# Optimization experiments

Hardware: AMD Instinct MI355X
Metric: run time of the kernel (lower is better)

## Reference

```python
import jax, jax.numpy as jnp
import numpy as np

D_MODEL = 1024
N_HEADS = 16
D_HEAD = D_MODEL // N_HEADS
CHUNK = 128
DECAY_RATE = 0.9


def setup_inputs() -> dict:
    key = jax.random.key(0)
    ks = jax.random.split(key, 10)
    B, L, D = 4, 4096, D_MODEL
    s = 1.0 / np.sqrt(D)
    return {
        "x": jax.random.normal(ks[0], (B, L, D), dtype=jnp.float32),
        "Wq": jax.random.normal(ks[1], (D, D), dtype=jnp.float32) * s,
        "bq": jnp.zeros((D,), dtype=jnp.float32),
        "Wk": jax.random.normal(ks[2], (D, D), dtype=jnp.float32) * s,
        "bk": jnp.zeros((D,), dtype=jnp.float32),
        "Wv": jax.random.normal(ks[3], (D, D), dtype=jnp.float32) * s,
        "bv": jnp.zeros((D,), dtype=jnp.float32),
        "Wo": jax.random.normal(ks[4], (D, D), dtype=jnp.float32) * s,
        "bo": jnp.zeros((D,), dtype=jnp.float32),
        "decay": jnp.full((N_HEADS,), DECAY_RATE, dtype=jnp.float32),
    }


def _retention(x, Wq, bq, Wk, bk, Wv, bv, Wo, bo, decay):
    B, L, D = x.shape
    H, Dh, C = N_HEADS, D_HEAD, CHUNK
    nC = L // C
    scale = Dh ** -0.5

    def split_heads(y):
        # [B,L,D] -> [nC, B, H, C, Dh]
        y = y.reshape(B, nC, C, H, Dh)
        return jnp.transpose(y, (1, 0, 3, 2, 4))

    q = split_heads(x @ Wq + bq)
    k = split_heads(x @ Wk + bk)
    v = split_heads(x @ Wv + bv)

    # per-head decay^position factor for query positions within a chunk: [H, C]
    pos = jnp.arange(C, dtype=jnp.float32)
    decay_fac = decay[:, None] ** pos[None, :]

    def step(carry, inp):
        pk, pv = carry            # [B,H,Dh] carried last k/v token
        qc, kc, vc = inp          # [B,H,C,Dh]
        kf = jnp.concatenate([pk[:, :, None], kc], axis=2)  # [B,H,C+1,Dh]
        vf = jnp.concatenate([pv[:, :, None], vc], axis=2)
        scores = jnp.einsum("bhqd,bhkd->bhqk", qc, kf) * scale
        scores = scores * decay_fac[None, :, :, None]
        attn = jax.nn.softmax(scores, axis=-1)
        out = jnp.einsum("bhqk,bhkd->bhqd", attn, vf)
        new_carry = (jax.lax.stop_gradient(kf[:, :, -1]),
                     jax.lax.stop_gradient(vf[:, :, -1]))
        return new_carry, out

    init = (jnp.zeros((B, H, Dh), x.dtype), jnp.zeros((B, H, Dh), x.dtype))
    _, ys = jax.lax.scan(step, init, (q, k, v))  # ys: [nC,B,H,C,Dh]
    out = jnp.transpose(ys, (1, 0, 3, 2, 4)).reshape(B, L, D)
    return out @ Wo + bo


def reference(x, Wq, bq, Wk, bk, Wv, bv, Wo, bo, decay):
    return _retention(x, Wq, bq, Wk, bk, Wv, bv, Wo, bo, decay)
```

## Files before the change

### kernel.cpp

```cpp
#include <hip/hip_runtime.h>

typedef unsigned short u16;
typedef unsigned int   u32;
typedef unsigned long long u64;

typedef __attribute__((ext_vector_type(8))) __bf16 bf16x8;
typedef __attribute__((ext_vector_type(4))) float  floatx4;

#define D_MODEL 1024
#define L_SEQ   4096
#define BATCH   4
#define N_HEADS 16
#define D_HEAD  64
#define CHUNK   128
#define N_CHUNKS 32
#define M_ROWS  (BATCH * L_SEQ)
#define NQKV    3072

__device__ __forceinline__ float bf2f(u16 u) {
    union { u32 i; float f; } x; x.i = ((u32)u) << 16; return x.f;
}
__device__ __forceinline__ u16 f2bf(float f) {
    union { u32 i; float fl; } x; x.fl = f;
    u32 i = x.i;
    u32 r = (i + 0x7FFFu + ((i >> 16) & 1u)) >> 16;
    return (u16)r;
}

__device__ __forceinline__ float load_decay(const void* dec, int h) {
    const u16* d16 = (const u16*)dec;
    const float as_bf = bf2f(d16[0]);
    if (as_bf > 1e-6f && as_bf <= 1.0001f) return bf2f(d16[h]);
    return ((const float*)dec)[h];
}

__device__ __forceinline__ void gload_lds16(const u16* g, u16* l) {
    __builtin_amdgcn_global_load_lds(
        (const __attribute__((address_space(1))) u32*)g,
        (__attribute__((address_space(3))) u32*)l, 16, 0, 0);
}

__global__ void detect_dtypes(const void* __restrict__ x,
                              const void* __restrict__ w,
                              int* __restrict__ flags) {
    const int lane = threadIdx.x;
    const u16* x16 = (const u16*)x;
    const u16* w16 = (const u16*)w;
    const float vx = fabsf(bf2f(x16[lane]));
    const float vw = fabsf(bf2f(w16[lane]));
    const bool ox = (vx != 0.0f) && (vx > 1e4f || vx < 1e-4f);
    const bool ow = (vw != 0.0f) && (vw > 1e4f || vw < 1e-4f);
    const u64 bx = __ballot(ox);
    const u64 bw = __ballot(ow);
    if (lane == 0) {
        flags[0] = (__popcll(bx) >= 8) ? 1 : 0;
        flags[1] = (__popcll(bw) >= 8) ? 1 : 0;
    }
}

__global__ __launch_bounds__(256)
void convert_x(const void* __restrict__ x, const int* __restrict__ flags,
               u16* __restrict__ xb) {
    const int mode = flags[0];
    const size_t i0 = ((size_t)blockIdx.x * 256 + threadIdx.x) * 8;
    if (mode) {
        const float* xf = (const float*)x;
        u16 tmp[8];
#pragma unroll
        for (int j = 0; j < 8; j++) tmp[j] = f2bf(xf[i0 + j]);
        *(uint4*)(xb + i0) = *(const uint4*)tmp;
    } else {
        *(uint4*)(xb + i0) = *(const uint4*)((const u16*)x + i0);
    }
}

__global__ __launch_bounds__(256)
void transpose4(const void* __restrict__ W0, const void* __restrict__ W1,
                const void* __restrict__ W2, const void* __restrict__ W3,
                const int* __restrict__ flags,
                u16* __restrict__ T0, u16* __restrict__ T1,
                u16* __restrict__ T2, u16* __restrict__ T3) {
    __shared__ u16 tile[32][33];
    const int mode = flags[1];
    const void* src; u16* dst;
    switch (blockIdx.z) {
        case 0: src = W0; dst = T0; break;
        case 1: src = W1; dst = T1; break;
        case 2: src = W2; dst = T2; break;
        default: src = W3; dst = T3; break;
    }
    const int tx = threadIdx.x & 31, ty = threadIdx.x >> 5;
    const int x0 = blockIdx.x * 32, y0 = blockIdx.y * 32;
#pragma unroll
    for (int i = 0; i < 32; i += 8) {
        const size_t idx = (size_t)(y0 + ty + i) * D_MODEL + x0 + tx;
        tile[ty + i][tx] = mode ? f2bf(((const float*)src)[idx])
                                : ((const u16*)src)[idx];
    }
    __syncthreads();
#pragma unroll
    for (int i = 0; i < 32; i += 8)
        dst[(size_t)(x0 + ty + i) * D_MODEL + y0 + tx] = tile[tx][ty + i];
}

__global__ __launch_bounds__(256)
void concat_bias(const void* __restrict__ bq, const void* __restrict__ bk,
                 const void* __restrict__ bv, const void* __restrict__ bo,
                 const int* __restrict__ flags, u16* __restrict__ dst) {
    const int i = blockIdx.x * 256 + threadIdx.x;
    const int mode = flags[1];
    const int which = i >> 10, idx = i & 1023;
    const void* src = (which == 0) ? bq : (which == 1) ? bk
                      : (which == 2) ? bv : bo;
    dst[i] = mode ? f2bf(((const float*)src)[idx]) : ((const u16*)src)[idx];
}

template <typename OutT>
__global__ __launch_bounds__(256)
void gemm_glds(const u16* __restrict__ A, const u16* __restrict__ Bt,
               const u16* __restrict__ bias, OutT* __restrict__ C, int N) {
    constexpr int K = 1024;
    __shared__ u16 sm[2 * 128 * 32];
    u16* As = sm;
    u16* Bs = sm + 128 * 32;

    const int t = threadIdx.x;
    const int lane = t & 63, w = t >> 6;
    const int col16 = lane & 15, quad = lane >> 4;
    const int wm = w >> 1, wn = w & 1;

    const int id = blockIdx.x;
    const int xcd = id & 7;
    const int s = id >> 3;
    const int g = xcd * 16 + (s & 15);
    const int x = s >> 4;
    const int m0 = g * 128, n0 = x * 128;

    const int srow = lane >> 2;
    const int sseg = lane & 3;
    const u16* Ab = A  + (size_t)(m0 + w * 16 + srow) * K + sseg * 8;
    const u16* Bb = Bt + (size_t)(n0 + w * 16 + srow) * K + sseg * 8;
    u16* AsW0 = &As[(w * 16) * 32];
    u16* AsW1 = &As[(w * 16 + 64) * 32];
    u16* BsW0 = &Bs[(w * 16) * 32];
    u16* BsW1 = &Bs[(w * 16 + 64) * 32];
    const size_t roff = (size_t)64 * K;

    floatx4 acc[4][4];
#pragma unroll
    for (int i = 0; i < 4; i++)
#pragma unroll
        for (int j = 0; j < 4; j++)
            acc[i][j] = floatx4{0.f, 0.f, 0.f, 0.f};

    for (int k0 = 0; k0 < K; k0 += 32) {
        __syncthreads();
        gload_lds16(Ab + k0, AsW0);
        gload_lds16(Ab + roff + k0, AsW1);
        gload_lds16(Bb + k0, BsW0);
        gload_lds16(Bb + roff + k0, BsW1);
        __syncthreads();

        bf16x8 af[4], bfr[4];
#pragma unroll
        for (int i = 0; i < 4; i++)
            af[i] = *(const bf16x8*)(&As[(wm * 64 + i * 16 + col16) * 32 + quad * 8]);
#pragma unroll
        for (int j = 0; j < 4; j++)
            bfr[j] = *(const bf16x8*)(&Bs[(wn * 64 + j * 16 + col16) * 32 + quad * 8]);
#pragma unroll
        for (int i = 0; i < 4; i++)
#pragma unroll
            for (int j = 0; j < 4; j++)
                acc[i][j] = __builtin_amdgcn_mfma_f32_16x16x32_bf16(
                    af[i], bfr[j], acc[i][j], 0, 0, 0);
    }

    if constexpr (sizeof(OutT) == 2) {
#pragma unroll
        for (int pass = 0; pass < 2; pass++) {
            __syncthreads();
            if (wm == pass) {
#pragma unroll
                for (int j = 0; j < 4; j++) {
                    const int lc = wn * 64 + j * 16 + col16;
                    const float bsf = bf2f(bias[n0 + lc]);
#pragma unroll
                    for (int i = 0; i < 4; i++)
#pragma unroll
                        for (int r = 0; r < 4; r++)
                            sm[(i * 16 + quad * 4 + r) * 128 + lc] =
                                f2bf(acc[i][j][r] + bsf);
                }
            }
            __syncthreads();
#pragma unroll
            for (int it = 0; it < 4; it++) {
                const int lin = it * 256 + t;
                const int row = lin >> 4, seg = lin & 15;
                *(uint4*)&C[(size_t)(m0 + pass * 64 + row) * N + n0 + seg * 8] =
                    *(const uint4*)&sm[row * 128 + seg * 8];
            }
        }
    } else {
#pragma unroll
        for (int j = 0; j < 4; j++) {
            const int gc = n0 + wn * 64 + j * 16 + col16;
            const float bsf = bf2f(bias[gc]);
#pragma unroll
            for (int i = 0; i < 4; i++) {
                const int gr = m0 + wm * 64 + i * 16 + quad * 4;
#pragma unroll
                for (int r = 0; r < 4; r++)
                    C[(size_t)(gr + r) * N + gc] = acc[i][j][r] + bsf;
            }
        }
    }
}

#define QS 72
#define PS 136
#define VT 136
#define KS_OFF (128 * QS)

__global__ __launch_bounds__(256)
void retention_mfma(const u16* __restrict__ qkv, const void* __restrict__ dec,
                    u16* __restrict__ att) {
    __shared__ u16 qk[2 * 128 * QS];
    __shared__ u16 vt[64 * VT];
    __shared__ float kp[64], vp[64], s0f[128];
    u16* Ps = qk;

    const int c = blockIdx.x, b = blockIdx.y, h = blockIdx.z;
    const int t = threadIdx.x;
    const int lane = t & 63, w = t >> 6;
    const int col16 = lane & 15, quad = lane >> 4;
    const int R0 = w * 32;
    const size_t base  = ((size_t)b * L_SEQ) * NQKV + h * D_HEAD;
    const size_t gbase = base + (size_t)(c * CHUNK) * NQKV;
    const size_t obase = (((size_t)b * L_SEQ) + c * CHUNK) * D_MODEL + h * D_HEAD;

#pragma unroll
    for (int it = 0; it < 4; it++) {
        const int i = it * 256 + t;
        const int row = i >> 3, seg = i & 7;
        const size_t go = gbase + (size_t)row * NQKV + seg * 8;
        *(uint4*)&qk[row * QS + seg * 8]          = *(const uint4*)(qkv + go);
        *(uint4*)&qk[KS_OFF + row * QS + seg * 8] = *(const uint4*)(qkv + go + 1024);
    }
#pragma unroll
    for (int it = 0; it < 4; it++) {
        const int i = it * 256 + t;
        const int key = i & 127, dseg = i >> 7;
        u16 tmp[8];
        *(uint4*)tmp = *(const uint4*)(qkv + gbase + (size_t)key * NQKV + 2048 + dseg * 8);
#pragma unroll
        for (int j = 0; j < 8; j++)
            vt[(dseg * 8 + j) * VT + key] = tmp[j];
    }
    if (t < 64) {
        const int gl = c * CHUNK - 1;
        float kpv = 0.f, vpv = 0.f;
        if (gl >= 0) {
            const size_t go = base + (size_t)gl * NQKV + t;
            kpv = bf2f(qkv[go + 1024]);
            vpv = bf2f(qkv[go + 2048]);
        }
        kp[t] = kpv; vp[t] = vpv;
    }
    __syncthreads();

    {
        const int row = t >> 1, half = t & 1;
        const u16* qrow = &qk[row * QS + half * 32];
        float s = 0.f;
#pragma unroll
        for (int d = 0; d < 32; d++) s += bf2f(qrow[d]) * kp[half * 32 + d];
        s += __shfl_xor(s, 1, 64);
        if (half == 0) s0f[row] = s;
    }
    __syncthreads();

    floatx4 accs[2][8];
#pragma unroll
    for (int rt = 0; rt < 2; rt++)
#pragma unroll
        for (int ct = 0; ct < 8; ct++)
            accs[rt][ct] = floatx4{0.f, 0.f, 0.f, 0.f};

#pragma unroll
    for (int k0 = 0; k0 < 2; k0++) {
        bf16x8 af0 = *(const bf16x8*)&qk[(R0 + col16) * QS + k0 * 32 + quad * 8];
        bf16x8 af1 = *(const bf16x8*)&qk[(R0 + 16 + col16) * QS + k0 * 32 + quad * 8];
#pragma unroll
        for (int ct = 0; ct < 8; ct++) {
            bf16x8 bfr = *(const bf16x8*)&qk[KS_OFF + (ct * 16 + col16) * QS + k0 * 32 + quad * 8];
            accs[0][ct] = __builtin_amdgcn_mfma_f32_16x16x32_bf16(af0, bfr, accs[0][ct], 0, 0, 0);
            accs[1][ct] = __builtin_amdgcn_mfma_f32_16x16x32_bf16(af1, bfr, accs[1][ct], 0, 0, 0);
        }
    }
    __syncthreads();

    const float dval = load_decay(dec, h);
    const float logd = __logf(dval);
    float p0v[2][4], invv[2][4];
#pragma unroll
    for (int rt = 0; rt < 2; rt++) {
#pragma unroll
        for (int r = 0; r < 4; r++) {
            const int row = R0 + rt * 16 + quad * 4 + r;
            const float dp = __expf((float)row * logd) * 0.125f;
            const float s0p = s0f[row] * dp;
            float vals[8];
            float vmax = s0p;
#pragma unroll
            for (int ct = 0; ct < 8; ct++) {
                vals[ct] = accs[rt][ct][r] * dp;
                vmax = fmaxf(vmax, vals[ct]);
            }
#pragma unroll
            for (int off = 1; off < 16; off <<= 1)
                vmax = fmaxf(vmax, __shfl_xor(vmax, off, 64));
            float lsum = 0.f;
#pragma unroll
            for (int ct = 0; ct < 8; ct++) {
                const float e = __expf(vals[ct] - vmax);
                lsum += e;
                Ps[row * PS + ct * 16 + col16] = f2bf(e);
            }
#pragma unroll
            for (int off = 1; off < 16; off <<= 1)
                lsum += __shfl_xor(lsum, off, 64);
            const float p0 = __expf(s0p - vmax);
            p0v[rt][r] = p0;
            invv[rt][r] = 1.0f / (lsum + p0);
        }
    }

    floatx4 acco[2][4];
#pragma unroll
    for (int rt = 0; rt < 2; rt++)
#pragma unroll
        for (int nt = 0; nt < 4; nt++)
            acco[rt][nt] = floatx4{0.f, 0.f, 0.f, 0.f};

#pragma unroll
    for (int k0 = 0; k0 < 4; k0++) {
        bf16x8 af0 = *(const bf16x8*)&Ps[(R0 + col16) * PS + k0 * 32 + quad * 8];
        bf16x8 af1 = *(const bf16x8*)&Ps[(R0 + 16 + col16) * PS + k0 * 32 + quad * 8];
#pragma unroll
        for (int nt = 0; nt < 4; nt++) {
            bf16x8 bfr = *(const bf16x8*)&vt[(nt * 16 + col16) * VT + k0 * 32 + quad * 8];
            acco[0][nt] = __builtin_amdgcn_mfma_f32_16x16x32_bf16(af0, bfr, acco[0][nt], 0, 0, 0);
            acco[1][nt] = __builtin_amdgcn_mfma_f32_16x16x32_bf16(af1, bfr, acco[1][nt], 0, 0, 0);
        }
    }

#pragma unroll
    for (int nt = 0; nt < 4; nt++) {
        const int gcol = nt * 16 + col16;
        const float vpc = vp[gcol];
#pragma unroll
        for (int rt = 0; rt < 2; rt++) {
#pragma unroll
            for (int r = 0; r < 4; r++) {
                const int row = R0 + rt * 16 + quad * 4 + r;
                const float val = (acco[rt][nt][r] + p0v[rt][r] * vpc) * invv[rt][r];
                att[obase + (size_t)row * D_MODEL + gcol] = f2bf(val);
            }
        }
    }
}

extern "C" void kernel_launch(void* const* d_in, const int* in_sizes, int n_in,
                              void* d_out, int out_size, void* d_ws, size_t ws_size,
                              hipStream_t stream) {
    const void* x   = d_in[0];
    const void* Wq  = d_in[1];
    const void* bq  = d_in[2];
    const void* Wk  = d_in[3];
    const void* bk  = d_in[4];
    const void* Wv  = d_in[5];
    const void* bv  = d_in[6];
    const void* Wo  = d_in[7];
    const void* bo  = d_in[8];
    const void* dec = d_in[9];
    float* out = (float*)d_out;

    char* ws = (char*)d_ws;
    const size_t mat = (size_t)M_ROWS * D_MODEL * sizeof(u16);
    const size_t wsz = (size_t)D_MODEL * D_MODEL * sizeof(u16);
    u16* xb   = (u16*)(ws);
    u16* qkv  = (u16*)(ws + mat);
    u16* WT   = (u16*)(ws + 4 * mat);
    u16* WoT  = WT + 3 * (size_t)D_MODEL * D_MODEL;
    u16* bias = (u16*)(ws + 4 * mat + 4 * wsz);
    int* flags = (int*)(ws + 4 * mat + 4 * wsz + 8192);

    dim3 tb(256);
    detect_dtypes<<<1, 64, 0, stream>>>(x, Wq, flags);
    convert_x<<<8192, tb, 0, stream>>>(x, flags, xb);
    transpose4<<<dim3(32, 32, 4), tb, 0, stream>>>(
        Wq, Wk, Wv, Wo, flags,
        WT, WT + wsz / 2, WT + wsz, WoT);
    concat_bias<<<16, tb, 0, stream>>>(bq, bk, bv, bo, flags, bias);
    gemm_glds<u16><<<24 * 128, tb, 0, stream>>>(xb, WT, bias, qkv, NQKV);
    retention_mfma<<<dim3(N_CHUNKS, BATCH, N_HEADS), tb, 0, stream>>>(qkv, dec, xb);
    gemm_glds<float><<<8 * 128, tb, 0, stream>>>(xb, WoT, bias + 3072, out, D_MODEL);
}
```

Before: 387.0 us.

## Replace 128x128 GEMM with 256x256 double-buffered 8-wave GEMM

Swaps the QKV and output-projection GEMMs from 128x128 tiles with 256 threads to 256x256 tiles with 512 threads and 128KB of dynamic LDS. Each K=64 step is double-buffered and split into quadrant sub-steps that interleave global-to-LDS prefetch with MFMA work. LDS uses XOR swizzling against bank conflicts, and MFMA sections raise wave priority with setprio. The aim is more data reuse per tile and hiding memory latency. The cost is fewer workgroups (768 and 256), one workgroup per CU, and heavier register pressure.

```diff
diff --git a/kernel.cpp b/kernel.cpp
--- a/kernel.cpp
+++ b/kernel.cpp
@@ -116,105 +116,170 @@
 }
 
 template <typename OutT>
-__global__ __launch_bounds__(256)
-void gemm_glds(const u16* __restrict__ A, const u16* __restrict__ Bt,
-               const u16* __restrict__ bias, OutT* __restrict__ C, int N) {
-    constexpr int K = 1024;
-    __shared__ u16 sm[2 * 128 * 32];
-    u16* As = sm;
-    u16* Bs = sm + 128 * 32;
+__global__ __launch_bounds__(512)
+void gemm_256(const u16* __restrict__ A, const u16* __restrict__ Bt,
+              const u16* __restrict__ bias, OutT* __restrict__ C, int N) {
+    extern __shared__ u16 lds[];
+    constexpr int K  = 1024;
+    constexpr int NT = K / 64;
 
     const int t = threadIdx.x;
     const int lane = t & 63, w = t >> 6;
     const int col16 = lane & 15, quad = lane >> 4;
-    const int wm = w >> 1, wn = w & 1;
-
-    const int id = blockIdx.x;
-    const int xcd = id & 7;
-    const int s = id >> 3;
-    const int g = xcd * 16 + (s & 15);
-    const int x = s >> 4;
-    const int m0 = g * 128, n0 = x * 128;
-
-    const int srow = lane >> 2;
-    const int sseg = lane & 3;
-    const u16* Ab = A  + (size_t)(m0 + w * 16 + srow) * K + sseg * 8;
-    const u16* Bb = Bt + (size_t)(n0 + w * 16 + srow) * K + sseg * 8;
-    u16* AsW0 = &As[(w * 16) * 32];
-    u16* AsW1 = &As[(w * 16 + 64) * 32];
-    u16* BsW0 = &Bs[(w * 16) * 32];
-    u16* BsW1 = &Bs[(w * 16 + 64) * 32];
-    const size_t roff = (size_t)64 * K;
-
-    floatx4 acc[4][4];
-#pragma unroll
-    for (int i = 0; i < 4; i++)
-#pragma unroll
-        for (int j = 0; j < 4; j++)
-            acc[i][j] = floatx4{0.f, 0.f, 0.f, 0.f};
-
-    for (int k0 = 0; k0 < K; k0 += 32) {
-        __syncthreads();
-        gload_lds16(Ab + k0, AsW0);
-        gload_lds16(Ab + roff + k0, AsW1);
-        gload_lds16(Bb + k0, BsW0);
-        gload_lds16(Bb + roff + k0, BsW1);
-        __syncthreads();
-
-        bf16x8 af[4], bfr[4];
+    const int wm = w >> 2, wn = w & 3;
+
+    const int nwg = gridDim.x;
+    const int chunk = nwg >> 3;
+    const int wg = (blockIdx.x & 7) * chunk + (blockIdx.x >> 3);
+    const int m0 = (wg & 63) * 256;
+    const int n0 = (wg >> 6) * 256;
+
+    const int rl = lane >> 3;
+    const int sp = lane & 7;
+    const int sseg = sp ^ rl;
+
+    auto STAGE_A = [&](int kt, int half) {
+        u16* l0 = lds + (kt & 1) * 32768 + (half * 128 + w * 8) * 64;
+        const u16* g0 = A + (size_t)(m0 + half * 128 + w * 8 + rl) * K
+                          + kt * 64 + sseg * 8;
+        gload_lds16(g0, l0);
+        gload_lds16(g0 + (size_t)64 * K, l0 + 64 * 64);
+    };
+    auto STAGE_B = [&](int kt, int half) {
+        u16* l0 = lds + (kt & 1) * 32768 + 16384 + (half * 128 + w * 8) * 64;
+        const u16* g0 = Bt + (size_t)(n0 + half * 128 + w * 8 + rl) * K
+                           + kt * 64 + sseg * 8;
+        gload_lds16(g0, l0);
+        gload_lds16(g0 + (size_t)64 * K, l0 + 64 * 64);
+    };
+
+    bf16x8 af[4][2], bfr[2][2];
+    floatx4 acc[2][2][4][2];
+#pragma unroll
+    for (int a = 0; a < 2; a++)
+#pragma unroll
+        for (int b = 0; b < 2; b++)
+#pragma unroll
+            for (int i = 0; i < 4; i++)
+#pragma unroll
+                for (int j = 0; j < 2; j++)
+                    acc[a][b][i][j] = floatx4{0.f, 0.f, 0.f, 0.f};
+
+    auto LDA = [&](int cur, int mh) {
+        const u16* tb = lds + cur * 32768;
+        const int rbase = mh * 128 + wm * 64 + col16;
+#pragma unroll
+        for (int i = 0; i < 4; i++) {
+            const int row = rbase + i * 16;
+#pragma unroll
+            for (int k0 = 0; k0 < 2; k0++) {
+                const int seg = (k0 * 4 + quad) ^ (row & 7);
+                af[i][k0] = *(const bf16x8*)(tb + row * 64 + seg * 8);
+            }
+        }
+    };
+    auto LDB = [&](int cur, int nh) {
+        const u16* tb = lds + cur * 32768 + 16384;
+        const int rbase = nh * 128 + wn * 32 + col16;
+#pragma unroll
+        for (int j = 0; j < 2; j++) {
+            const int row = rbase + j * 16;
+#pragma unroll
+            for (int k0 = 0; k0 < 2; k0++) {
+                const int seg = (k0 * 4 + quad) ^ (row & 7);
+                bfr[j][k0] = *(const bf16x8*)(tb + row * 64 + seg * 8);
+            }
+        }
+    };
+    auto MMQ = [&](floatx4 (&aq)[4][2]) {
+        __builtin_amdgcn_s_setprio(1);
 #pragma unroll
         for (int i = 0; i < 4; i++)
-            af[i] = *(const bf16x8*)(&As[(wm * 64 + i * 16 + col16) * 32 + quad * 8]);
-#pragma unroll
-        for (int j = 0; j < 4; j++)
-            bfr[j] = *(const bf16x8*)(&Bs[(wn * 64 + j * 16 + col16) * 32 + quad * 8]);
-#pragma unroll
-        for (int i = 0; i < 4; i++)
-#pragma unroll
-            for (int j = 0; j < 4; j++)
-                acc[i][j] = __builtin_amdgcn_mfma_f32_16x16x32_bf16(
-                    af[i], bfr[j], acc[i][j], 0, 0, 0);
+#pragma unroll
+            for (int j = 0; j < 2; j++)
+#pragma unroll
+                for (int k0 = 0; k0 < 2; k0++)
+                    aq[i][j] = __builtin_amdgcn_mfma_f32_16x16x32_bf16(
+                        af[i][k0], bfr[j][k0], aq[i][j], 0, 0, 0);
+        __builtin_amdgcn_s_setprio(0);
+    };
+
+    STAGE_A(0, 0); STAGE_B(0, 0); STAGE_A(0, 1); STAGE_B(0, 1);
+    STAGE_A(1, 0); STAGE_B(1, 1);
+    asm volatile("s_waitcnt vmcnt(4)" ::: "memory");
+    __builtin_amdgcn_s_barrier();
+
+    for (int kt = 0; kt < NT; ++kt) {
+        const int cur = kt & 1;
+        LDA(cur, 0); LDB(cur, 0);
+        if (kt + 1 < NT) STAGE_A(kt + 1, 1);
+        __builtin_amdgcn_s_barrier();
+        MMQ(acc[0][0]);
+        __builtin_amdgcn_s_barrier();
+        LDB(cur, 1);
+        if (kt + 1 < NT) STAGE_B(kt + 1, 0);
+        __builtin_amdgcn_s_barrier();
+        MMQ(acc[0][1]);
+        __builtin_amdgcn_s_barrier();
+        LDA(cur, 1);
+        if (kt + 2 < NT) STAGE_A(kt + 2, 0);
+        __builtin_amdgcn_s_barrier();
+        MMQ(acc[1][1]);
+        __builtin_amdgcn_s_barrier();
+        LDB(cur, 0);
+        if (kt + 2 < NT) STAGE_B(kt + 2, 1);
+        __builtin_amdgcn_s_barrier();
+        MMQ(acc[1][0]);
+        if (kt + 2 < NT) asm volatile("s_waitcnt vmcnt(4)" ::: "memory");
+        else             asm volatile("s_waitcnt vmcnt(0)" ::: "memory");
+        __builtin_amdgcn_s_barrier();
     }
 
     if constexpr (sizeof(OutT) == 2) {
-#pragma unroll
-        for (int pass = 0; pass < 2; pass++) {
+        u16* sm = lds;
+#pragma unroll
+        for (int mh = 0; mh < 2; mh++) {
             __syncthreads();
-            if (wm == pass) {
-#pragma unroll
-                for (int j = 0; j < 4; j++) {
-                    const int lc = wn * 64 + j * 16 + col16;
-                    const float bsf = bf2f(bias[n0 + lc]);
+#pragma unroll
+            for (int nh = 0; nh < 2; nh++)
+#pragma unroll
+                for (int j = 0; j < 2; j++) {
+                    const int lcol = nh * 128 + wn * 32 + j * 16 + col16;
+                    const float bsf = bf2f(bias[n0 + lcol]);
 #pragma unroll
                     for (int i = 0; i < 4; i++)
 #pragma unroll
                         for (int r = 0; r < 4; r++)
-                            sm[(i * 16 + quad * 4 + r) * 128 + lc] =
-                                f2bf(acc[i][j][r] + bsf);
+                            sm[(wm * 64 + i * 16 + quad * 4 + r) * 264 + lcol] =
+                                f2bf(acc[mh][nh][i][j][r] + bsf);
                 }
-            }
             __syncthreads();
 #pragma unroll
-            for (int it = 0; it < 4; it++) {
-                const int lin = it * 256 + t;
-                const int row = lin >> 4, seg = lin & 15;
-                *(uint4*)&C[(size_t)(m0 + pass * 64 + row) * N + n0 + seg * 8] =
-                    *(const uint4*)&sm[row * 128 + seg * 8];
+            for (int it = 0; it < 8; it++) {
+                const int lin = it * 512 + t;
+                const int row = lin >> 5, seg = lin & 31;
+                *(uint4*)&C[(size_t)(m0 + mh * 128 + row) * N + n0 + seg * 8] =
+                    *(const uint4*)&sm[row * 264 + seg * 8];
             }
         }
     } else {
 #pragma unroll
-        for (int j = 0; j < 4; j++) {
-            const int gc = n0 + wn * 64 + j * 16 + col16;
-            const float bsf = bf2f(bias[gc]);
-#pragma unroll
-            for (int i = 0; i < 4; i++) {
-                const int gr = m0 + wm * 64 + i * 16 + quad * 4;
-#pragma unroll
-                for (int r = 0; r < 4; r++)
-                    C[(size_t)(gr + r) * N + gc] = acc[i][j][r] + bsf;
-            }
-        }
+        for (int mh = 0; mh < 2; mh++)
+#pragma unroll
+            for (int nh = 0; nh < 2; nh++)
+#pragma unroll
+                for (int j = 0; j < 2; j++) {
+                    const int gcol = n0 + nh * 128 + wn * 32 + j * 16 + col16;
+                    const float bsf = bf2f(bias[gcol]);
+#pragma unroll
+                    for (int i = 0; i < 4; i++) {
+                        const int gr = m0 + mh * 128 + wm * 64 + i * 16 + quad * 4;
+#pragma unroll
+                        for (int r = 0; r < 4; r++)
+                            C[(size_t)(gr + r) * N + gcol] =
+                                acc[mh][nh][i][j][r] + bsf;
+                    }
+                }
     }
 }
 
@@ -404,7 +469,9 @@
         Wq, Wk, Wv, Wo, flags,
         WT, WT + wsz / 2, WT + wsz, WoT);
     concat_bias<<<16, tb, 0, stream>>>(bq, bk, bv, bo, flags, bias);
-    gemm_glds<u16><<<24 * 128, tb, 0, stream>>>(xb, WT, bias, qkv, NQKV);
+    gemm_256<u16><<<dim3(64 * 12), dim3(512), 131072, stream>>>(
+        xb, WT, bias, qkv, NQKV);
     retention_mfma<<<dim3(N_CHUNKS, BATCH, N_HEADS), tb, 0, stream>>>(qkv, dec, xb);
-    gemm_glds<float><<<8 * 128, tb, 0, stream>>>(xb, WoT, bias + 3072, out, D_MODEL);
-}
+    gemm_256<float><<<dim3(64 * 4), dim3(512), 131072, stream>>>(
+        xb, WoT, bias + 3072, out, D_MODEL);
+}
```

Measured after the change: 349.3 us. 9.7% less time.
